# Kernel optimization log

Hardware: AMD Instinct MI355X
Metric: run time of the kernel (lower is better)

The kernel has to match this reference:

```python
import jax, jax.numpy as jnp
import numpy as np

L, B, S, D, H, F = 4, 8, 512, 512, 8, 2048
KS = (1, 3, 5)
DEPTH = D // H


def causal_conv(x, W, b):
    # x: [B,S,D], W: [k,D,D] (WIO), causal left pad k-1
    k = W.shape[0]
    y = jax.lax.conv_general_dilated(x, W, (1,), [(k - 1, 0)],
                                     dimension_numbers=('NWC', 'WIO', 'NWC'))
    return y + b


def layer_norm(x, g, b, eps=1e-6):
    mu = jnp.mean(x, -1, keepdims=True)
    var = jnp.mean((x - mu) ** 2, -1, keepdims=True)
    return (x - mu) * jax.lax.rsqrt(var + eps) * g + b


def split_heads(t):
    return t.reshape(B, S, H, DEPTH).transpose(0, 2, 1, 3)  # [B,H,S,depth]


def setup_inputs() -> dict:
    key = jax.random.key(0)
    keys = iter(jax.random.split(key, 16))
    rn = lambda shape, s=0.02: jax.random.normal(next(keys), shape, jnp.float32) * s
    inp = {"x": jax.random.normal(next(keys), (B, S, D), jnp.float32)}
    for k in KS:
        inp[f"Wq{k}"] = rn((L, k, D, D))
        inp[f"Wk{k}"] = rn((L, k, D, D))
    inp["bq"] = jnp.zeros((L, 3, D), jnp.float32)
    inp["bk"] = jnp.zeros((L, 3, D), jnp.float32)
    inp["Wv"] = rn((L, 3, 1, D, D))
    inp["bv"] = jnp.zeros((L, 3, D), jnp.float32)
    inp["Wo"] = rn((L, D, D)); inp["bo"] = jnp.zeros((L, D), jnp.float32)
    inp["W1"] = rn((L, D, F)); inp["b1"] = jnp.zeros((L, F), jnp.float32)
    inp["W2"] = rn((L, F, D)); inp["b2"] = jnp.zeros((L, D), jnp.float32)
    inp["ln1_g"] = jnp.ones((L, D), jnp.float32); inp["ln1_b"] = jnp.zeros((L, D), jnp.float32)
    inp["ln2_g"] = jnp.ones((L, D), jnp.float32); inp["ln2_b"] = jnp.zeros((L, D), jnp.float32)
    return inp


def reference(x, Wq1, Wq3, Wq5, Wk1, Wk3, Wk5, bq, bk, Wv, bv, Wo, bo,
              W1, b1, W2, b2, ln1_g, ln1_b, ln2_g, ln2_b):
    # causal look-ahead mask: 1 - band_part(ones, -1, 0), added as mask * -1e9
    neg_mask = (1.0 - jnp.tril(jnp.ones((S, S), jnp.float32))) * -1e9
    scale = 1.0 / jnp.sqrt(jnp.float32(DEPTH))
    Wqs, Wks = (Wq1, Wq3, Wq5), (Wk1, Wk3, Wk5)
    for l in range(L):
        outs = []
        for i in range(len(KS)):
            q = split_heads(causal_conv(x, Wqs[i][l], bq[l, i]))
            k = split_heads(causal_conv(x, Wks[i][l], bk[l, i]))
            v = split_heads(causal_conv(x, Wv[l, i], bv[l, i]))
            logits = jnp.einsum('bhqd,bhkd->bhqk', q, k) * scale + neg_mask
            a = jax.nn.softmax(logits, axis=-1)
            o = jnp.einsum('bhqk,bhkd->bhqd', a, v)
            outs.append(o.transpose(0, 2, 1, 3).reshape(B, S, D))
        attn_out = ((outs[0] + outs[1] + outs[2]) / 3.0) @ Wo[l] + bo[l]
        out1 = layer_norm(attn_out + x, ln1_g[l], ln1_b[l])
        ffn = jax.nn.relu(out1 @ W1[l] + b1[l]) @ W2[l] + b2[l]
        x = layer_norm(ffn + out1, ln2_g[l], ln2_b[l])
    return x
```

## Files before the change

kernel.cpp:

```cpp
#include <hip/hip_runtime.h>
#include <cstdint>
#include <cstddef>

#define Dm 512
#define Sm 512
#define Bm 8
#define Hm 8
#define Fm 2048
#define Mm 4096
#define Lm 4

typedef __bf16 bf16x8 __attribute__((ext_vector_type(8)));
typedef float  fx4    __attribute__((ext_vector_type(4)));
typedef float  fx2    __attribute__((ext_vector_type(2)));
typedef unsigned short u16;
typedef unsigned short u16x4 __attribute__((ext_vector_type(4)));
typedef short s16x8 __attribute__((ext_vector_type(8)));

__device__ __forceinline__ u16 f2b(float f) {
  union { float f; uint32_t u; } v; v.f = f;
  uint32_t u = v.u;
  return (u16)((u + 0x7fffu + ((u >> 16) & 1u)) >> 16);
}
__device__ __forceinline__ float b2f(u16 h) {
  union { uint32_t u; float f; } v; v.u = ((uint32_t)h) << 16;
  return v.f;
}

__device__ __forceinline__ void gload16(const void* g, void* l) {
  __builtin_amdgcn_global_load_lds(
      (const __attribute__((address_space(1))) void*)g,
      (__attribute__((address_space(3))) void*)l, 16, 0, 0);
}

__global__ void cast_bf16_kernel(const float* __restrict__ in, u16* __restrict__ out,
                                 u16* __restrict__ zpad, float* __restrict__ zerof) {
  int i = (blockIdx.x * 256 + threadIdx.x) * 4;
  fx4 v = *(const fx4*)(in + i);
  u16x4 o;
  #pragma unroll
  for (int j = 0; j < 4; ++j) o[j] = f2b(v[j]);
  *(u16x4*)(out + i) = o;
  if (blockIdx.x == 0) { zpad[threadIdx.x] = 0; zpad[threadIdx.x + 256] = 0; }
  if (blockIdx.x == 1) {
    #pragma unroll
    for (int j = 0; j < 8; ++j) zerof[threadIdx.x * 8 + j] = 0.f;
  }
}

__global__ void avg3_kernel(const u16* __restrict__ o3, u16* __restrict__ out) {
  int i = (blockIdx.x * 256 + threadIdx.x) * 4;
  u16x4 a = *(const u16x4*)(o3 + i);
  u16x4 b = *(const u16x4*)(o3 + (size_t)Mm*Dm + i);
  u16x4 c = *(const u16x4*)(o3 + (size_t)2*Mm*Dm + i);
  u16x4 r;
  #pragma unroll
  for (int j = 0; j < 4; ++j)
    r[j] = f2b((b2f(a[j]) + b2f(b[j]) + b2f(c[j])) * (1.f/3.f));
  *(u16x4*)(out + i) = r;
}

__global__ void ln_kernel(const float* __restrict__ in, const float* __restrict__ in2,
                          const float* __restrict__ gam, const float* __restrict__ bet,
                          float* __restrict__ outf, u16* __restrict__ outb) {
  int row = blockIdx.x;
  int t = threadIdx.x;
  const float* x = in + (size_t)row * Dm;
  fx4 v0 = *(const fx4*)(x + t*4);
  fx4 v1 = *(const fx4*)(x + 256 + t*4);
  if (in2) {
    const float* x2 = in2 + (size_t)row * Dm;
    fx4 w0 = *(const fx4*)(x2 + t*4);
    fx4 w1 = *(const fx4*)(x2 + 256 + t*4);
    #pragma unroll
    for (int j = 0; j < 4; ++j) { v0[j] += w0[j]; v1[j] += w1[j]; }
  }
  float s = 0.f, sq = 0.f;
  #pragma unroll
  for (int j = 0; j < 4; ++j) { s += v0[j] + v1[j]; sq += v0[j]*v0[j] + v1[j]*v1[j]; }
  #pragma unroll
  for (int off = 1; off < 64; off <<= 1) { s += __shfl_xor(s, off, 64); sq += __shfl_xor(sq, off, 64); }
  float mu  = s * (1.f/Dm);
  float var = sq * (1.f/Dm) - mu*mu;
  float rstd = rsqrtf(var + 1e-6f);
  fx4 g0 = *(const fx4*)(gam + t*4), g1 = *(const fx4*)(gam + 256 + t*4);
  fx4 b0 = *(const fx4*)(bet + t*4), b1 = *(const fx4*)(bet + 256 + t*4);
  float* of = outf + (size_t)row*Dm;
  u16*   ob = outb + (size_t)row*Dm;
  fx4 y0, y1; u16x4 h0, h1;
  #pragma unroll
  for (int j = 0; j < 4; ++j) {
    y0[j] = (v0[j]-mu)*rstd*g0[j] + b0[j];
    y1[j] = (v1[j]-mu)*rstd*g1[j] + b1[j];
    h0[j] = f2b(y0[j]); h1[j] = f2b(y1[j]);
  }
  *(fx4*)(of + t*4) = y0; *(fx4*)(of + 256 + t*4) = y1;
  *(u16x4*)(ob + t*4) = h0; *(u16x4*)(ob + 256 + t*4) = h1;
}

#define TST 130
__global__ void prep_kernel(u16* __restrict__ packed,
    const float* __restrict__ Wq1, const float* __restrict__ Wq3, const float* __restrict__ Wq5,
    const float* __restrict__ Wk1, const float* __restrict__ Wk3, const float* __restrict__ Wk5,
    const float* __restrict__ Wv,  const float* __restrict__ Wo,
    const float* __restrict__ W1,  const float* __restrict__ W2, int layer) {
  __shared__ float T[64 * TST];
  constexpr int t0[13] = {0,32,128,288,320,416,576,608,640,672,704,832,960};
  int bid = blockIdx.x;
  int seg = 0;
  while (bid >= t0[seg+1]) ++seg;
  int local = bid - t0[seg];
  const float* src; int K, N;
  switch (seg) {
    case 0:  src = Wq1 + (size_t)layer*512*512;   K = 512;  N = 512;  break;
    case 1:  src = Wq3 + (size_t)layer*3*512*512; K = 1536; N = 512;  break;
    case 2:  src = Wq5 + (size_t)layer*5*512*512; K = 2560; N = 512;  break;
    case 3:  src = Wk1 + (size_t)layer*512*512;   K = 512;  N = 512;  break;
    case 4:  src = Wk3 + (size_t)layer*3*512*512; K = 1536; N = 512;  break;
    case 5:  src = Wk5 + (size_t)layer*5*512*512; K = 2560; N = 512;  break;
    case 6:  src = Wv + (size_t)(layer*3+0)*512*512; K = 512; N = 512; break;
    case 7:  src = Wv + (size_t)(layer*3+1)*512*512; K = 512; N = 512; break;
    case 8:  src = Wv + (size_t)(layer*3+2)*512*512; K = 512; N = 512; break;
    case 9:  src = Wo + (size_t)layer*512*512;    K = 512;  N = 512;  break;
    case 10: src = W1 + (size_t)layer*512*2048;   K = 512;  N = 2048; break;
    default: src = W2 + (size_t)layer*2048*512;   K = 2048; N = 512;  break;
  }
  int KT = K >> 6;
  int ntile = local / KT, ktile = local - ntile*KT;
  const float* sb = src + (size_t)(ktile*64)*N + ntile*128;
  int tid = threadIdx.x;
  #pragma unroll
  for (int i = 0; i < 16; ++i) {
    int idx = i*256 + tid;
    int row = idx >> 6, col2 = (idx & 63) * 2;
    fx2 v = *(const fx2*)(sb + (size_t)row*N + col2);
    *(fx2*)(&T[row*TST + col2]) = v;
  }
  __syncthreads();
  u16* dst = packed + ((size_t)bid << 13);
  #pragma unroll
  for (int j = 0; j < 4; ++j) {
    int z = j*256 + tid;
    int row = z >> 3;
    int c = (z & 7) ^ (row & 7);
    s16x8 o;
    #pragma unroll
    for (int e = 0; e < 8; ++e) o[e] = (short)f2b(T[(c*8 + e)*TST + row]);
    *(s16x8*)(dst + z*8) = o;
  }
}

__global__ __launch_bounds__(256, 3) void conv_all(const u16* __restrict__ xb,
    const u16* __restrict__ packed,
    const float* __restrict__ bq, const float* __restrict__ bk, const float* __restrict__ bv,
    u16* __restrict__ qb, u16* __restrict__ kb, u16* __restrict__ vT, int layer,
    const u16* __restrict__ zpad) {
  __shared__ __align__(16) u16 As[2][8192];
  constexpr int t0c[9]   = {0,32,128,288,320,416,576,608,640};
  constexpr int tapsc[9] = {1,3,5,1,3,5,1,1,1};
  constexpr int order[9] = {2,5,1,4,0,3,6,7,8};
  int bid = blockIdx.x;
  int unit = order[bid >> 7];
  int local = bid & 127;
  int mtile = local >> 2, ntile = local & 3;
  int taps = tapsc[unit];
  int brow = mtile * 128, bcol = ntile * 128;
  int tid = threadIdx.x, lane = tid & 63, wid = tid >> 6;
  int wm = wid >> 1, wn = wid & 1;
  int r16 = lane & 15, g = lane >> 4;
  int tbase = t0c[unit] + ntile * taps * 8;
  fx4 acc[4][4] = {};
  int ntiles = taps * 8;
  int st = 0, skt = 0;
  auto stageA = [&](int bufi) {
    int shift = taps - 1 - st;
    int c0 = skt << 6;
    #pragma unroll
    for (int j = 0; j < 4; ++j) {
      int zb = wid*256 + j*64;
      int zz = zb + lane;
      int row = zz >> 3, c = (zz & 7) ^ (row & 7);
      int s = (brow + row) & (Sm - 1);
      const u16* src = (s >= shift) ? (xb + (size_t)(brow + row - shift)*Dm + c0 + c*8) : zpad;
      gload16(src, &As[bufi][zb * 8]);
    }
  };
  stageA(0);
  ++skt; if (skt == 8) { skt = 0; ++st; }
  __syncthreads();
  for (int idx = 0; idx < ntiles; ++idx) {
    int cur = idx & 1;
    const u16* wtc = packed + ((size_t)(tbase + idx) << 13);
    bf16x8 b[2][4];
    #pragma unroll
    for (int kk = 0; kk < 2; ++kk)
      #pragma unroll
      for (int n = 0; n < 4; ++n) {
        int row = wn*64 + n*16 + r16;
        b[kk][n] = *(const bf16x8*)(wtc + (row << 6) + (((kk*4 + g) ^ (row & 7)) << 3));
      }
    if (idx + 1 < ntiles) {
      stageA(cur ^ 1);
      ++skt; if (skt == 8) { skt = 0; ++st; }
    }
    bf16x8 a[2][4];
    #pragma unroll
    for (int kk = 0; kk < 2; ++kk)
      #pragma unroll
      for (int m = 0; m < 4; ++m) {
        int row = wm*64 + m*16 + r16;
        a[kk][m] = *(const bf16x8*)(&As[cur][(row << 6) + (((kk*4 + g) ^ (row & 7)) << 3)]);
      }
    #pragma unroll
    for (int kk = 0; kk < 2; ++kk)
      #pragma unroll
      for (int m = 0; m < 4; ++m)
        #pragma unroll
        for (int n = 0; n < 4; ++n)
          acc[m][n] = __builtin_amdgcn_mfma_f32_16x16x32_bf16(a[kk][m], b[kk][n], acc[m][n], 0, 0, 0);
    __syncthreads();
  }
  const float* bias; u16* outp;
  if (unit < 3)      { bias = bq + (size_t)(layer*3 + unit)*Dm;   outp = qb + (size_t)unit*Mm*Dm; }
  else if (unit < 6) { bias = bk + (size_t)(layer*3 + unit-3)*Dm; outp = kb + (size_t)(unit-3)*Mm*Dm; }
  else               { bias = bv + (size_t)(layer*3 + unit-6)*Dm; outp = vT + ((size_t)(unit-6) << 21); }
  if (unit < 6) {
    #pragma unroll
    for (int m = 0; m < 4; ++m) {
      int row0 = brow + wm*64 + m*16 + g*4;
      #pragma unroll
      for (int n = 0; n < 4; ++n) {
        int col = bcol + wn*64 + n*16 + r16;
        float bv_ = bias[col];
        #pragma unroll
        for (int r = 0; r < 4; ++r)
          outp[(size_t)(row0 + r)*Dm + col] = f2b(acc[m][n][r] + bv_);
      }
    }
  } else {
    #pragma unroll
    for (int m = 0; m < 4; ++m) {
      int row0 = brow + wm*64 + m*16 + g*4;
      int bidx = row0 >> 9, spos = row0 & 511;
      #pragma unroll
      for (int n = 0; n < 4; ++n) {
        int col = bcol + wn*64 + n*16 + r16;
        int hh = col >> 6, dd = col & 63;
        float bv_ = bias[col];
        u16x4 pk;
        #pragma unroll
        for (int r = 0; r < 4; ++r) pk[r] = f2b(acc[m][n][r] + bv_);
        *(u16x4*)(outp + (((size_t)(bidx*8 + hh)*64 + dd) << 9) + spos) = pk;
      }
    }
  }
}

template<int MODE, int BMt, int WN, bool CAUSAL>
__device__ __forceinline__ void gemm_core(const u16* __restrict__ A, int lda, int Ktap, int taps,
    const u16* __restrict__ Wt, const float* __restrict__ bias, const float* __restrict__ res,
    u16* __restrict__ outb, float* __restrict__ outf, int N, const u16* __restrict__ zpad,
    int ktN_stride, int ktile0) {
  constexpr int NR = 128 / (16 * WN);
  __shared__ __align__(16) u16 As[2][BMt * 64];
  int tid = threadIdx.x, lane = tid & 63, wid = tid >> 6;
  int wm = (WN == 2) ? (wid >> 1) : 0;
  int wn = (WN == 2) ? (wid & 1) : wid;
  int r16 = lane & 15, g = lane >> 4;
  int brow = blockIdx.x * BMt, bcol = blockIdx.y * 128;
  int KT = Ktap >> 6;
  const u16* WtN = Wt + ((size_t)(blockIdx.y * ktN_stride + ktile0) << 13);
  fx4 acc[4][NR] = {};
  int ntiles = taps * KT;
  int st = 0, skt = 0;
  auto stageA = [&](int bufi) {
    int shift = taps - 1 - st;
    int c0 = skt << 6;
    #pragma unroll
    for (int j = 0; j < BMt/32; ++j) {
      int zb = wid*(BMt*2) + j*64;
      int zz = zb + lane;
      int row = zz >> 3, c = (zz & 7) ^ (row & 7);
      const u16* src;
      if (CAUSAL) {
        int s = (brow + row) & (Sm - 1);
        src = (s >= shift) ? (A + (size_t)(brow + row - shift)*lda + c0 + c*8) : zpad;
      } else {
        src = A + (size_t)(brow + row)*lda + c0 + c*8;
      }
      gload16(src, &As[bufi][zb * 8]);
    }
  };
  stageA(0);
  ++skt; if (skt == KT) { skt = 0; ++st; }
  __syncthreads();
  for (int idx = 0; idx < ntiles; ++idx) {
    int cur = idx & 1;
    const u16* wtc = WtN + ((size_t)idx << 13);
    bf16x8 b[2][NR];
    #pragma unroll
    for (int kk = 0; kk < 2; ++kk)
      #pragma unroll
      for (int n = 0; n < NR; ++n) {
        int row = wn*(NR*16) + n*16 + r16;
        b[kk][n] = *(const bf16x8*)(wtc + (row << 6) + (((kk*4 + g) ^ (row & 7)) << 3));
      }
    if (idx + 1 < ntiles) {
      stageA(cur ^ 1);
      ++skt; if (skt == KT) { skt = 0; ++st; }
    }
    bf16x8 a[2][4];
    #pragma unroll
    for (int kk = 0; kk < 2; ++kk)
      #pragma unroll
      for (int m = 0; m < 4; ++m) {
        int row = wm*64 + m*16 + r16;
        a[kk][m] = *(const bf16x8*)(&As[cur][(row << 6) + (((kk*4 + g) ^ (row & 7)) << 3)]);
      }
    #pragma unroll
    for (int kk = 0; kk < 2; ++kk)
      #pragma unroll
      for (int m = 0; m < 4; ++m)
        #pragma unroll
        for (int n = 0; n < NR; ++n)
          acc[m][n] = __builtin_amdgcn_mfma_f32_16x16x32_bf16(a[kk][m], b[kk][n], acc[m][n], 0, 0, 0);
    __syncthreads();
  }
  #pragma unroll
  for (int m = 0; m < 4; ++m) {
    int row0 = brow + wm*64 + m*16 + g*4;
    #pragma unroll
    for (int n = 0; n < NR; ++n) {
      int col = bcol + wn*(NR*16) + n*16 + r16;
      float bv_ = bias[col];
      #pragma unroll
      for (int r = 0; r < 4; ++r) {
        size_t idx = (size_t)(row0 + r)*N + col;
        float v = acc[m][n][r] + bv_;
        if (MODE == 0)      outb[idx] = f2b(v);
        else if (MODE == 1) outb[idx] = f2b(fmaxf(v, 0.f));
        else                outf[idx] = v + (res ? res[idx] : 0.f);
      }
    }
  }
}

template<int MODE, int BMt, int WN, int LB>
__global__ __launch_bounds__(256, LB) void gemm_dense(const u16* __restrict__ A, int lda, int K,
    const u16* __restrict__ Wt, const float* __restrict__ bias, const float* __restrict__ res,
    u16* __restrict__ outb, float* __restrict__ outf, int N) {
  gemm_core<MODE, BMt, WN, false>(A, lda, K, 1, Wt, bias, res, outb, outf, N, nullptr, K >> 6, 0);
}

__global__ __launch_bounds__(256, 3) void gemm_ffn2(const u16* __restrict__ A,
    const u16* __restrict__ Wt, const float* __restrict__ bias, const float* __restrict__ zerof,
    const float* __restrict__ res, float* __restrict__ pre, float* __restrict__ pre2) {
  int z = blockIdx.z;
  gemm_core<2, 64, 4, false>(A + z*1024, 2048, 1024, 1, Wt,
      z ? zerof : bias, z ? nullptr : res, nullptr, z ? pre2 : pre, 512, nullptr, 32, z*16);
}

__global__ __launch_bounds__(256, 3) void attn_kernel(const u16* __restrict__ qb,
    const u16* __restrict__ kb, const u16* __restrict__ vTb, u16* __restrict__ ob) {
  __shared__ __align__(16) u16 Ks[2][4096];
  __shared__ __align__(16) u16 Vs[2][4096];
  __shared__ __align__(16) u16 Ps[4][1024];
  int a = blockIdx.x, bh = blockIdx.y, br = blockIdx.z;
  int b = bh >> 3, h = bh & 7;
  const u16* q  = qb + (size_t)br*Mm*Dm;
  const u16* k  = kb + (size_t)br*Mm*Dm;
  const u16* vT = vTb + (((size_t)br << 21) + ((size_t)bh << 15));
  u16* o = ob + (size_t)br*Mm*Dm;
  int tid = threadIdx.x, lane = tid & 63, wid = tid >> 6;
  int r16 = lane & 15, g = lane >> 4;
  size_t rowbase = (size_t)b * Sm;
  int qt[2] = {7 - a, a};
  int nkt = qt[0] + 1;

  bf16x8 qa[2][2];
  #pragma unroll
  for (int t2 = 0; t2 < 2; ++t2)
    #pragma unroll
    for (int c = 0; c < 2; ++c)
      qa[t2][c] = *(const bf16x8*)(q + (rowbase + qt[t2]*64 + wid*16 + r16)*Dm + h*64 + c*32 + g*8);

  float m_[2][4], l_[2][4];
  fx4 accO[2][4] = {};
  #pragma unroll
  for (int t2 = 0; t2 < 2; ++t2)
    #pragma unroll
    for (int r = 0; r < 4; ++r) { m_[t2][r] = -3.0e38f; l_[t2][r] = 0.f; }

  auto stage = [&](int kt, int bufi) {
    #pragma unroll
    for (int it = 0; it < 2; ++it) {
      int zb = wid*128 + it*64;
      int zz = zb + lane;
      int row = zz >> 3, c = (zz & 7) ^ (row & 7);
      gload16(k + (rowbase + kt*64 + row)*Dm + h*64 + c*8, &Ks[bufi][zb * 8]);
      gload16(vT + ((size_t)row << 9) + kt*64 + c*8, &Vs[bufi][zb * 8]);
    }
  };
  stage(0, 0);
  __syncthreads();

  for (int kt = 0; kt < nkt; ++kt) {
    int cur = kt & 1;
    if (kt + 1 < nkt) stage(kt + 1, cur ^ 1);
    #pragma unroll
    for (int t2 = 0; t2 < 2; ++t2) {
      if (t2 == 0 || kt <= qt[1]) {
        fx4 sacc[4] = {};
        #pragma unroll
        for (int c = 0; c < 2; ++c)
          #pragma unroll
          for (int n = 0; n < 4; ++n) {
            int row = n*16 + r16;
            bf16x8 kf = *(const bf16x8*)(&Ks[cur][(row << 6) + (((c*4 + g) ^ (row & 7)) << 3)]);
            sacc[n] = __builtin_amdgcn_mfma_f32_16x16x32_bf16(qa[t2][c], kf, sacc[n], 0, 0, 0);
          }
        float sv[4][4];
        bool diag = (kt == qt[t2]);
        #pragma unroll
        for (int n = 0; n < 4; ++n)
          #pragma unroll
          for (int r = 0; r < 4; ++r) {
            float s = sacc[n][r] * 0.125f;
            if (diag && (n*16 + r16 > wid*16 + g*4 + r)) s = -3.0e38f;
            sv[n][r] = s;
          }
        #pragma unroll
        for (int r = 0; r < 4; ++r) {
          float rm = fmaxf(fmaxf(sv[0][r], sv[1][r]), fmaxf(sv[2][r], sv[3][r]));
          #pragma unroll
          for (int off = 1; off < 16; off <<= 1) rm = fmaxf(rm, __shfl_xor(rm, off, 64));
          float mnew = fmaxf(m_[t2][r], rm);
          float corr = __expf(m_[t2][r] - mnew);
          m_[t2][r] = mnew;
          float rs = 0.f;
          #pragma unroll
          for (int n = 0; n < 4; ++n) { float p = __expf(sv[n][r] - mnew); sv[n][r] = p; rs += p; }
          #pragma unroll
          for (int off = 1; off < 16; off <<= 1) rs += __shfl_xor(rs, off, 64);
          l_[t2][r] = l_[t2][r]*corr + rs;
          #pragma unroll
          for (int n = 0; n < 4; ++n) accO[t2][n][r] *= corr;
        }
        #pragma unroll
        for (int n = 0; n < 4; ++n)
          #pragma unroll
          for (int r = 0; r < 4; ++r) {
            int qq = g*4 + r;
            Ps[wid][(qq << 6) + (((n*2 + (r16 >> 3)) ^ (qq & 7)) << 3) + (r16 & 7)] = f2b(sv[n][r]);
          }
        #pragma unroll
        for (int kk = 0; kk < 2; ++kk) {
          bf16x8 pa = *(const bf16x8*)(&Ps[wid][(r16 << 6) + (((kk*4 + g) ^ (r16 & 7)) << 3)]);
          #pragma unroll
          for (int n = 0; n < 4; ++n) {
            int row = n*16 + r16;
            bf16x8 vf = *(const bf16x8*)(&Vs[cur][(row << 6) + (((kk*4 + g) ^ (row & 7)) << 3)]);
            accO[t2][n] = __builtin_amdgcn_mfma_f32_16x16x32_bf16(pa, vf, accO[t2][n], 0, 0, 0);
          }
        }
      }
    }
    __syncthreads();
  }
  #pragma unroll
  for (int t2 = 0; t2 < 2; ++t2)
    #pragma unroll
    for (int n = 0; n < 4; ++n)
      #pragma unroll
      for (int r = 0; r < 4; ++r) {
        int qrow = qt[t2]*64 + wid*16 + g*4 + r;
        o[(rowbase + qrow)*Dm + h*64 + n*16 + r16] = f2b(accO[t2][n][r] / l_[t2][r]);
      }
}

extern "C" void kernel_launch(void* const* d_in, const int* in_sizes, int n_in,
                              void* d_out, int out_size, void* d_ws, size_t ws_size,
                              hipStream_t stream) {
  const float* x_in = (const float*)d_in[0];
  const float* Wq1 = (const float*)d_in[1];
  const float* Wk1 = (const float*)d_in[2];
  const float* Wq3 = (const float*)d_in[3];
  const float* Wk3 = (const float*)d_in[4];
  const float* Wq5 = (const float*)d_in[5];
  const float* Wk5 = (const float*)d_in[6];
  const float* bq  = (const float*)d_in[7];
  const float* bk  = (const float*)d_in[8];
  const float* Wv  = (const float*)d_in[9];
  const float* bv  = (const float*)d_in[10];
  const float* Wo  = (const float*)d_in[11];
  const float* bo  = (const float*)d_in[12];
  const float* W1  = (const float*)d_in[13];
  const float* b1  = (const float*)d_in[14];
  const float* W2  = (const float*)d_in[15];
  const float* b2  = (const float*)d_in[16];
  const float* ln1g = (const float*)d_in[17];
  const float* ln1b = (const float*)d_in[18];
  const float* ln2g = (const float*)d_in[19];
  const float* ln2b = (const float*)d_in[20];

  char* ws = (char*)d_ws;
  size_t off = 0;
  auto alloc = [&](size_t bytes) { void* p = ws + off; off += (bytes + 255) & ~(size_t)255; return p; };
  float* x_f32 = (float*)alloc((size_t)Mm*Dm*4);
  u16*   xb    = (u16*)  alloc((size_t)Mm*Dm*2);
  u16*   qbuf  = (u16*)  alloc((size_t)3*Mm*Dm*2);
  u16*   kbuf  = (u16*)  alloc((size_t)3*Mm*Dm*2);
  u16*   vT    = (u16*)  alloc((size_t)3*Mm*Dm*2);
  u16*   obuf  = (u16*)  alloc((size_t)3*Mm*Dm*2);
  u16*   avgb  = (u16*)  alloc((size_t)Mm*Dm*2);
  float* pre   = (float*)alloc((size_t)Mm*Dm*4);
  float* pre2  = (float*)alloc((size_t)Mm*Dm*4);
  float* out1f = (float*)alloc((size_t)Mm*Dm*4);
  u16*   out1b = (u16*)  alloc((size_t)Mm*Dm*2);
  u16*   midb  = (u16*)  alloc((size_t)Mm*Fm*2);
  u16*   packed= (u16*)  alloc((size_t)960*8192*2);
  u16*   zpad  = (u16*)  alloc(1024);
  float* zerof = (float*)alloc(2048*4);

  cast_bf16_kernel<<<2048, 256, 0, stream>>>(x_in, xb, zpad, zerof);
  for (int l = 0; l < Lm; ++l) {
    const float* xs = (l == 0) ? x_in : x_f32;
    prep_kernel<<<960, 256, 0, stream>>>(packed, Wq1, Wq3, Wq5, Wk1, Wk3, Wk5,
                                         Wv, Wo, W1, W2, l);
    conv_all<<<1152, 256, 0, stream>>>(
        xb, packed, bq, bk, bv, qbuf, kbuf, vT, l, zpad);
    attn_kernel<<<dim3(4, 64, 3), 256, 0, stream>>>(qbuf, kbuf, vT, obuf);
    avg3_kernel<<<2048, 256, 0, stream>>>(obuf, avgb);
    gemm_dense<2, 64, 4, 3><<<dim3(64, 4), 256, 0, stream>>>(
        avgb, 512, 512, packed + ((size_t)672 << 13), bo + (size_t)l*Dm, xs, nullptr, pre, 512);
    ln_kernel<<<4096, 64, 0, stream>>>(pre, nullptr, ln1g + (size_t)l*Dm, ln1b + (size_t)l*Dm,
                                       out1f, out1b);
    gemm_dense<1, 128, 2, 3><<<dim3(32, 16), 256, 0, stream>>>(
        out1b, 512, 512, packed + ((size_t)704 << 13), b1 + (size_t)l*Fm, nullptr, midb, nullptr, 2048);
    gemm_ffn2<<<dim3(64, 4, 2), 256, 0, stream>>>(
        midb, packed + ((size_t)832 << 13), b2 + (size_t)l*Dm, zerof, out1f, pre, pre2);
    float* lnout = (l == Lm-1) ? (float*)d_out : x_f32;
    ln_kernel<<<4096, 64, 0, stream>>>(pre, pre2, ln2g + (size_t)l*Dm, ln2b + (size_t)l*Dm,
                                       lnout, xb);
  }
}
```

Baseline: 671.4 us.

## Use explicit vmcnt waits and MFMA priority in GEMMs; drop FFN2 split-K

The GEMM main loops in the conv and dense kernels now use explicit s_waitcnt vmcnt counts and a bare s_barrier instead of __syncthreads. This lets the next tile's global-to-LDS loads stay in flight while the current tile is computed. The MFMA block is wrapped in s_setprio to favour the compute waves. The FFN2 split-K over two blocks (pre plus pre2 partials) is replaced by a single dense GEMM over K=2048, which removes the pre2 buffer and the extra add in the LN kernel but gives fewer blocks and a longer K loop. The hand-tuned vmcnt counts must match the exact number of outstanding loads, or the code reads LDS tiles before they arrive.

```diff
diff --git a/kernel.cpp b/kernel.cpp
--- a/kernel.cpp
+++ b/kernel.cpp
@@ -33,8 +33,17 @@
       (__attribute__((address_space(3))) void*)l, 16, 0, 0);
 }
 
+template<int N>
+__device__ __forceinline__ void vwait() {
+  if constexpr (N == 4)       asm volatile("s_waitcnt vmcnt(4)" ::: "memory");
+  else if constexpr (N == 6)  asm volatile("s_waitcnt vmcnt(6)" ::: "memory");
+  else if constexpr (N == 8)  asm volatile("s_waitcnt vmcnt(8)" ::: "memory");
+  else if constexpr (N == 12) asm volatile("s_waitcnt vmcnt(12)" ::: "memory");
+  else                        asm volatile("s_waitcnt vmcnt(0)" ::: "memory");
+}
+
 __global__ void cast_bf16_kernel(const float* __restrict__ in, u16* __restrict__ out,
-                                 u16* __restrict__ zpad, float* __restrict__ zerof) {
+                                 u16* __restrict__ zpad) {
   int i = (blockIdx.x * 256 + threadIdx.x) * 4;
   fx4 v = *(const fx4*)(in + i);
   u16x4 o;
@@ -42,10 +51,6 @@
   for (int j = 0; j < 4; ++j) o[j] = f2b(v[j]);
   *(u16x4*)(out + i) = o;
   if (blockIdx.x == 0) { zpad[threadIdx.x] = 0; zpad[threadIdx.x + 256] = 0; }
-  if (blockIdx.x == 1) {
-    #pragma unroll
-    for (int j = 0; j < 8; ++j) zerof[threadIdx.x * 8 + j] = 0.f;
-  }
 }
 
 __global__ void avg3_kernel(const u16* __restrict__ o3, u16* __restrict__ out) {
@@ -199,9 +204,13 @@
         int row = wn*64 + n*16 + r16;
         b[kk][n] = *(const bf16x8*)(wtc + (row << 6) + (((kk*4 + g) ^ (row & 7)) << 3));
       }
-    if (idx + 1 < ntiles) {
+    bool staged = (idx + 1 < ntiles);
+    if (staged) {
       stageA(cur ^ 1);
       ++skt; if (skt == 8) { skt = 0; ++st; }
+      vwait<12>();
+    } else {
+      vwait<8>();
     }
     bf16x8 a[2][4];
     #pragma unroll
@@ -211,6 +220,7 @@
         int row = wm*64 + m*16 + r16;
         a[kk][m] = *(const bf16x8*)(&As[cur][(row << 6) + (((kk*4 + g) ^ (row & 7)) << 3)]);
       }
+    __builtin_amdgcn_s_setprio(1);
     #pragma unroll
     for (int kk = 0; kk < 2; ++kk)
       #pragma unroll
@@ -218,7 +228,8 @@
         #pragma unroll
         for (int n = 0; n < 4; ++n)
           acc[m][n] = __builtin_amdgcn_mfma_f32_16x16x32_bf16(a[kk][m], b[kk][n], acc[m][n], 0, 0, 0);
-    __syncthreads();
+    __builtin_amdgcn_s_setprio(0);
+    __builtin_amdgcn_s_barrier();
   }
   const float* bias; u16* outp;
   if (unit < 3)      { bias = bq + (size_t)(layer*3 + unit)*Dm;   outp = qb + (size_t)unit*Mm*Dm; }
@@ -262,6 +273,8 @@
     u16* __restrict__ outb, float* __restrict__ outf, int N, const u16* __restrict__ zpad,
     int ktN_stride, int ktile0) {
   constexpr int NR = 128 / (16 * WN);
+  constexpr int BL = 2 * NR;
+  constexpr int AD = BMt / 32;
   __shared__ __align__(16) u16 As[2][BMt * 64];
   int tid = threadIdx.x, lane = tid & 63, wid = tid >> 6;
   int wm = (WN == 2) ? (wid >> 1) : 0;
@@ -277,7 +290,7 @@
     int shift = taps - 1 - st;
     int c0 = skt << 6;
     #pragma unroll
-    for (int j = 0; j < BMt/32; ++j) {
+    for (int j = 0; j < AD; ++j) {
       int zb = wid*(BMt*2) + j*64;
       int zz = zb + lane;
       int row = zz >> 3, c = (zz & 7) ^ (row & 7);
@@ -305,9 +318,13 @@
         int row = wn*(NR*16) + n*16 + r16;
         b[kk][n] = *(const bf16x8*)(wtc + (row << 6) + (((kk*4 + g) ^ (row & 7)) << 3));
       }
-    if (idx + 1 < ntiles) {
+    bool staged = (idx + 1 < ntiles);
+    if (staged) {
       stageA(cur ^ 1);
       ++skt; if (skt == KT) { skt = 0; ++st; }
+      vwait<BL + AD>();
+    } else {
+      vwait<BL>();
     }
     bf16x8 a[2][4];
     #pragma unroll
@@ -317,6 +334,7 @@
         int row = wm*64 + m*16 + r16;
         a[kk][m] = *(const bf16x8*)(&As[cur][(row << 6) + (((kk*4 + g) ^ (row & 7)) << 3)]);
       }
+    __builtin_amdgcn_s_setprio(1);
     #pragma unroll
     for (int kk = 0; kk < 2; ++kk)
       #pragma unroll
@@ -324,7 +342,8 @@
         #pragma unroll
         for (int n = 0; n < NR; ++n)
           acc[m][n] = __builtin_amdgcn_mfma_f32_16x16x32_bf16(a[kk][m], b[kk][n], acc[m][n], 0, 0, 0);
-    __syncthreads();
+    __builtin_amdgcn_s_setprio(0);
+    __builtin_amdgcn_s_barrier();
   }
   #pragma unroll
   for (int m = 0; m < 4; ++m) {
@@ -350,14 +369,6 @@
     const u16* __restrict__ Wt, const float* __restrict__ bias, const float* __restrict__ res,
     u16* __restrict__ outb, float* __restrict__ outf, int N) {
   gemm_core<MODE, BMt, WN, false>(A, lda, K, 1, Wt, bias, res, outb, outf, N, nullptr, K >> 6, 0);
-}
-
-__global__ __launch_bounds__(256, 3) void gemm_ffn2(const u16* __restrict__ A,
-    const u16* __restrict__ Wt, const float* __restrict__ bias, const float* __restrict__ zerof,
-    const float* __restrict__ res, float* __restrict__ pre, float* __restrict__ pre2) {
-  int z = blockIdx.z;
-  gemm_core<2, 64, 4, false>(A + z*1024, 2048, 1024, 1, Wt,
-      z ? zerof : bias, z ? nullptr : res, nullptr, z ? pre2 : pre, 512, nullptr, 32, z*16);
 }
 
 __global__ __launch_bounds__(256, 3) void attn_kernel(const u16* __restrict__ qb,
@@ -514,15 +525,13 @@
   u16*   obuf  = (u16*)  alloc((size_t)3*Mm*Dm*2);
   u16*   avgb  = (u16*)  alloc((size_t)Mm*Dm*2);
   float* pre   = (float*)alloc((size_t)Mm*Dm*4);
-  float* pre2  = (float*)alloc((size_t)Mm*Dm*4);
   float* out1f = (float*)alloc((size_t)Mm*Dm*4);
   u16*   out1b = (u16*)  alloc((size_t)Mm*Dm*2);
   u16*   midb  = (u16*)  alloc((size_t)Mm*Fm*2);
   u16*   packed= (u16*)  alloc((size_t)960*8192*2);
   u16*   zpad  = (u16*)  alloc(1024);
-  float* zerof = (float*)alloc(2048*4);
-
-  cast_bf16_kernel<<<2048, 256, 0, stream>>>(x_in, xb, zpad, zerof);
+
+  cast_bf16_kernel<<<2048, 256, 0, stream>>>(x_in, xb, zpad);
   for (int l = 0; l < Lm; ++l) {
     const float* xs = (l == 0) ? x_in : x_f32;
     prep_kernel<<<960, 256, 0, stream>>>(packed, Wq1, Wq3, Wq5, Wk1, Wk3, Wk5,
@@ -537,10 +546,10 @@
                                        out1f, out1b);
     gemm_dense<1, 128, 2, 3><<<dim3(32, 16), 256, 0, stream>>>(
         out1b, 512, 512, packed + ((size_t)704 << 13), b1 + (size_t)l*Fm, nullptr, midb, nullptr, 2048);
-    gemm_ffn2<<<dim3(64, 4, 2), 256, 0, stream>>>(
-        midb, packed + ((size_t)832 << 13), b2 + (size_t)l*Dm, zerof, out1f, pre, pre2);
+    gemm_dense<2, 64, 4, 3><<<dim3(64, 4), 256, 0, stream>>>(
+        midb, 2048, 2048, packed + ((size_t)832 << 13), b2 + (size_t)l*Dm, out1f, nullptr, pre, 512);
     float* lnout = (l == Lm-1) ? (float*)d_out : x_f32;
-    ln_kernel<<<4096, 64, 0, stream>>>(pre, pre2, ln2g + (size_t)l*Dm, ln2b + (size_t)l*Dm,
+    ln_kernel<<<4096, 64, 0, stream>>>(pre, nullptr, ln2g + (size_t)l*Dm, ln2b + (size_t)l*Dm,
                                        lnout, xb);
   }
 }
```

Result: slower. 686.7 us (+2.3%).
